# Kernel tuning notes

Measured on AMD Instinct MI355X. Metric: run time of the kernel, lower is better.

## Reference

```python
import jax, jax.numpy as jnp
import numpy as np

B, CIN, T = 32, 16, 4096
H, DEPTH, E, K = 192, 4, 4, 7
DILATIONS = (1, 2, 4, 8)
NUM_BANDS, P = 16, 8
HM = 2 * H  # mlp_ratio = 2.0
NCLS = 50
GAIN_LIMIT = 0.5
EPS = 1e-5


def _rbf_basis(num_bins, num_bands):
    freqs = jnp.linspace(0.0, 1.0, num_bins)
    centers = jnp.linspace(0.0, 1.0, num_bands)
    width = 1.5 / (num_bands - 1)
    basis = jnp.exp(-0.5 * ((freqs[None, :] - centers[:, None]) / width) ** 2)
    return basis / jnp.clip(basis.sum(-1, keepdims=True), 1e-8)


def _layernorm(x, g, b):
    m = x.mean(-1, keepdims=True)
    v = x.var(-1, keepdims=True)
    return (x - m) / jnp.sqrt(v + EPS) * g + b


def _groupnorm1(x, g, b):
    # GroupNorm(1, C): normalize over (C, T) per sample, per-channel affine
    m = x.mean((1, 2), keepdims=True)
    v = x.var((1, 2), keepdims=True)
    return (x - m) / jnp.sqrt(v + EPS) * g[None, :, None] + b[None, :, None]


def _bn_eval(x, g, b):
    # eval-mode BatchNorm1d with running_mean=0, running_var=1
    return x * (g / jnp.sqrt(1.0 + EPS))[None, :, None] + b[None, :, None]


def _gelu(x):
    return jax.nn.gelu(x, approximate=False)


def _dwconv(x, w, dilation):
    pad = (K // 2) * dilation
    return jax.lax.conv_general_dilated(
        x, w, (1,), [(pad, pad)], rhs_dilation=(dilation,),
        dimension_numbers=("NCH", "OIH", "NCH"), feature_group_count=x.shape[1])


def setup_inputs() -> dict:
    key = jax.random.key(0)
    ks = jax.random.split(key, 12)
    return {
        "x": jax.random.normal(ks[0], (B, CIN, T), jnp.float32),
        "stem_w": jax.random.normal(ks[1], (H, CIN, 3)) * 0.1,
        "stem_bn_g": jnp.ones((H,)), "stem_bn_b": jnp.zeros((H,)),
        "ln_g": jnp.ones((NUM_BANDS,)), "ln_b": jnp.zeros((NUM_BANDS,)),
        "proj_w": jax.random.normal(ks[2], (NUM_BANDS, NUM_BANDS)) * 0.25,
        "prototypes": jax.random.normal(ks[3], (P, NUM_BANDS)) * 0.02,
        "route_lib": jax.random.normal(ks[4], (P, DEPTH, E)) * 0.1,
        "gain_lib": jax.random.normal(ks[5], (P, DEPTH, H)) * 0.1,
        "norm1_g": jnp.ones((DEPTH, H)), "norm1_b": jnp.zeros((DEPTH, H)),
        "expert_w": jax.random.normal(ks[6], (DEPTH, E, H, 1, K)) * 0.2,
        "mix_w": jax.random.normal(ks[7], (DEPTH, H, H)) * (1.0 / np.sqrt(H)),
        "mix_bn_g": jnp.ones((DEPTH, H)), "mix_bn_b": jnp.zeros((DEPTH, H)),
        "norm2_g": jnp.ones((DEPTH, H)), "norm2_b": jnp.zeros((DEPTH, H)),
        "mlp_w1": jax.random.normal(ks[8], (DEPTH, HM, H)) * (1.0 / np.sqrt(H)),
        "mlp_b1": jnp.zeros((DEPTH, HM)),
        "mlp_w2": jax.random.normal(ks[9], (DEPTH, H, HM)) * (1.0 / np.sqrt(HM)),
        "mlp_b2": jnp.zeros((DEPTH, H)),
        "head_w": jax.random.normal(ks[10], (NCLS, H)) * (1.0 / np.sqrt(H)),
        "head_b": jnp.zeros((NCLS,)),
    }


def reference(x, stem_w, stem_bn_g, stem_bn_b, ln_g, ln_b, proj_w, prototypes,
              route_lib, gain_lib, norm1_g, norm1_b, expert_w, mix_w, mix_bn_g,
              mix_bn_b, norm2_g, norm2_b, mlp_w1, mlp_b1, mlp_w2, mlp_b2,
              head_w, head_b):
    # --- SpectralSummary ---
    spec = jnp.fft.rfft(x.astype(jnp.float32), axis=-1, norm="ortho")
    mag = jnp.abs(spec).mean(axis=1)                      # [B, bins]
    basis = _rbf_basis(mag.shape[-1], NUM_BANDS)          # [bands, bins]
    summary = jnp.log1p(mag) @ basis.T                    # [B, bands]
    # --- PrototypeRouter ---
    s = _layernorm(summary, ln_g, ln_b)
    rs = s @ proj_w.T
    logits = -((rs[:, None, :] - prototypes[None]) ** 2).mean(-1)  # [B, P]
    assign = jax.nn.softmax(logits * np.sqrt(NUM_BANDS), axis=-1)
    routes = jax.nn.softmax(jnp.einsum("bp,pde->bde", assign, route_lib), axis=-1)  # [B,D,E]
    gains = 1.0 + GAIN_LIMIT * jnp.tanh(jnp.einsum("bp,pdc->bdc", assign, gain_lib))  # [B,D,C]
    # --- Backbone stem ---
    z = jax.lax.conv_general_dilated(x, stem_w, (1,), [(1, 1)],
                                     dimension_numbers=("NCH", "OIH", "NCH"))
    z = _gelu(_bn_eval(z, stem_bn_g, stem_bn_b))
    # --- Routed temporal blocks ---
    for d in range(DEPTH):
        zn = _groupnorm1(z, norm1_g[d], norm1_b[d])
        pieces = jnp.stack([_dwconv(zn, expert_w[d, e], DILATIONS[e]) for e in range(E)], axis=1)  # [B,E,C,T]
        mixed = jnp.einsum("be,bect->bct", routes[:, d], pieces)
        mixed = mixed * gains[:, d][:, :, None]
        mixed = _gelu(_bn_eval(jnp.einsum("oc,bct->bot", mix_w[d], mixed), mix_bn_g[d], mix_bn_b[d]))
        z = z + mixed
        zn2 = _groupnorm1(z, norm2_g[d], norm2_b[d])
        h = _gelu(jnp.einsum("oc,bct->bot", mlp_w1[d], zn2) + mlp_b1[d][None, :, None])
        z = z + jnp.einsum("oc,bct->bot", mlp_w2[d], h) + mlp_b2[d][None, :, None]
    # --- Head: global average pool + linear ---
    pooled = z.mean(-1)
    return pooled @ head_w.T + head_b
```

## Files before the change

### kernel.cpp

```cpp
#include <hip/hip_runtime.h>
#include <math.h>

constexpr int cB = 32, cCIN = 16, cT = 4096, cH = 192, cD = 4, cE = 4, cK = 7;
constexpr int cBANDS = 16, cP = 8, cHM = 384, cNCLS = 50, cBINS = 2049;
constexpr float cEPS = 1e-5f;
constexpr int TT = 64, HALO = 24;
constexpr int ZSTR = 112;
constexpr int NTAP = 19;
constexpr float INV_SQRT2 = 0.7071067811865475f;

typedef __bf16 bf16_t;
typedef bf16_t bf16x8 __attribute__((ext_vector_type(8)));
typedef float f32x4 __attribute__((ext_vector_type(4)));

constexpr int OFFS[NTAP] = {-24,-16,-12,-8,-6,-4,-3,-2,-1,0,1,2,3,4,6,8,12,16,24};
constexpr int IDXT[cE][cK] = {
    {6, 7, 8, 9, 10, 11, 12},
    {4, 5, 7, 9, 11, 13, 14},
    {2, 3, 5, 9, 13, 15, 16},
    {0, 1, 3, 9, 15, 17, 18}};

__device__ __forceinline__ int xcd_swz(int bid) {
    return (bid & 7) * 256 + (bid >> 3);
}

__device__ __forceinline__ float fast_erf(float x) {
    float ax = fabsf(x);
    float t = 1.0f / fmaf(0.3275911f, ax, 1.0f);
    float p = t * fmaf(t, fmaf(t, fmaf(t, fmaf(t, 1.061405429f, -1.453152027f),
                                       1.421413741f), -0.284496736f), 0.254829592f);
    float e = __expf(-ax * ax);
    float r = 1.0f - p * e;
    return copysignf(r, x);
}
__device__ __forceinline__ float gelu_exact(float v) {
    return 0.5f * v * (1.0f + fast_erf(v * INV_SQRT2));
}
__device__ __forceinline__ unsigned short f2bf(float f) {
    union { float f; unsigned u; } v; v.f = f;
    unsigned r = (v.u + 0x7FFFu + ((v.u >> 16) & 1u)) >> 16;
    return (unsigned short)r;
}
__device__ __forceinline__ float bf2f(unsigned short u) {
    union { unsigned u; float f; } v; v.u = ((unsigned)u) << 16;
    return v.f;
}
__device__ __forceinline__ float bflo(unsigned u) {
    union { unsigned u; float f; } v; v.u = u << 16;
    return v.f;
}
__device__ __forceinline__ float bfhi(unsigned u) {
    union { unsigned u; float f; } v; v.u = u & 0xFFFF0000u;
    return v.f;
}

__global__ __launch_bounds__(256) void k_zero(float* __restrict__ p, int n) {
    int i = blockIdx.x * 256 + threadIdx.x;
    if (i < n) p[i] = 0.f;
}

__global__ __launch_bounds__(256) void k_cvt(const float* __restrict__ src,
                                             unsigned short* __restrict__ dst, int n) {
    int i = blockIdx.x * 256 + threadIdx.x;
    if (i < n) dst[i] = f2bf(src[i]);
}

__global__ __launch_bounds__(256) void k_cvt_w2perm(const float* __restrict__ src,
                                                    unsigned short* __restrict__ dst, int n) {
    int j = blockIdx.x * 256 + threadIdx.x;
    if (j >= n) return;
    int dd = j / (cH * cHM);
    int rem = j % (cH * cHM);
    int o = rem / cHM, m = rem % cHM;
    int wid = m / 96;
    int rr = m % 96;
    int chunk = rr / 48;
    int ii = rr % 48;
    int pos = chunk * 192 + wid * 48 + ii;
    dst[(size_t)dd * cH * cHM + (size_t)o * cHM + pos] = f2bf(src[j]);
}

__global__ __launch_bounds__(256) void k_twiddle(float2* __restrict__ tw) {
    int ls = blockIdx.x;
    int n = cT >> ls;
    int cnt = n >> 1;
    int base = cT - (cT >> ls);
    for (int p = threadIdx.x; p < cnt; p += 256) {
        float ang = -6.283185307179586f * (float)p / (float)n;
        float sv, cv;
        sincosf(ang, &sv, &cv);
        tw[base + p] = make_float2(cv, sv);
    }
}

__global__ __launch_bounds__(256) void k_fft_mag(const float* __restrict__ x,
                                                 const float2* __restrict__ tw,
                                                 float* __restrict__ mag) {
    constexpr int N2 = cT / 2;
    __shared__ float Sr[2][N2];
    __shared__ float Si[2][N2];
    int b = blockIdx.x / cCIN, c = blockIdx.x % cCIN;
    const float* xp = x + ((size_t)b * cCIN + c) * cT;
#pragma unroll
    for (int it = 0; it < N2 / 256; it++) {
        int t = threadIdx.x + it * 256;
        float2 v = *reinterpret_cast<const float2*>(&xp[2 * t]);
        Sr[0][t] = v.x; Si[0][t] = v.y;
    }
    __syncthreads();
    int cur = 0;
    for (int ls = 0; ls < 11; ls++) {
        int s = 1 << ls;
        int twb = cT - (cT >> (ls + 1));
#pragma unroll
        for (int it = 0; it < N2 / 512; it++) {
            int j = threadIdx.x + it * 256;
            int p = j >> ls;
            float2 w = tw[twb + p];
            float wr = w.x, wi = w.y;
            int ia = j, ib = j + N2 / 2;
            float ar = Sr[cur][ia], ai = Si[cur][ia];
            float br = Sr[cur][ib], bi = Si[cur][ib];
            int oa = j + (j & ~(s - 1));
            int ob = oa + s;
            Sr[cur ^ 1][oa] = ar + br;
            Si[cur ^ 1][oa] = ai + bi;
            float tr = ar - br, ti = ai - bi;
            Sr[cur ^ 1][ob] = tr * wr - ti * wi;
            Si[cur ^ 1][ob] = tr * wi + ti * wr;
        }
        __syncthreads();
        cur ^= 1;
    }
    const float scale = (1.0f / 64.0f) * (1.0f / 16.0f);
    for (int k = threadIdx.x; k <= N2; k += 256) {
        int k2 = k & (N2 - 1), km = (N2 - k) & (N2 - 1);
        float yr = Sr[cur][k2], yi = Si[cur][k2];
        float zr = Sr[cur][km], zi = Si[cur][km];
        float Ar = 0.5f * (yr + zr), Ai = 0.5f * (yi - zi);
        float Br = 0.5f * (yi + zi), Bi = -0.5f * (yr - zr);
        float wr, wi;
        if (k < N2) { float2 w = tw[k]; wr = w.x; wi = w.y; }
        else { wr = -1.f; wi = 0.f; }
        float Xr = Ar + wr * Br - wi * Bi;
        float Xi = Ai + wr * Bi + wi * Br;
        atomicAdd(&mag[b * cBINS + k], sqrtf(Xr * Xr + Xi * Xi) * scale);
    }
}

__global__ __launch_bounds__(256) void k_basis(float* __restrict__ basis) {
    __shared__ float vals[cBINS];
    __shared__ float red[256];
    int band = blockIdx.x;
    float cb = (float)band / 15.0f;
    float inv_w = 15.0f / 1.5f;
    float local = 0.f;
    for (int k = threadIdx.x; k < cBINS; k += 256) {
        float f = (float)k / 2048.0f;
        float u = (f - cb) * inv_w;
        float v = expf(-0.5f * u * u);
        vals[k] = v;
        local += v;
    }
    red[threadIdx.x] = local;
    __syncthreads();
    for (int s = 128; s > 0; s >>= 1) {
        if (threadIdx.x < s) red[threadIdx.x] += red[threadIdx.x + s];
        __syncthreads();
    }
    float inv_sum = 1.0f / fmaxf(red[0], 1e-8f);
    for (int k = threadIdx.x; k < cBINS; k += 256)
        basis[band * cBINS + k] = vals[k] * inv_sum;
}

__global__ __launch_bounds__(256) void k_summary(const float* __restrict__ mag,
                                                 const float* __restrict__ basis,
                                                 float* __restrict__ summary) {
    int b = blockIdx.x;
    float acc[cBANDS];
#pragma unroll
    for (int i = 0; i < cBANDS; i++) acc[i] = 0.f;
    for (int k = threadIdx.x; k < cBINS; k += 256) {
        float lm = log1pf(mag[b * cBINS + k]);
#pragma unroll
        for (int band = 0; band < cBANDS; band++) acc[band] += lm * basis[band * cBINS + k];
    }
    __shared__ float red[cBANDS][256];
#pragma unroll
    for (int band = 0; band < cBANDS; band++) red[band][threadIdx.x] = acc[band];
    __syncthreads();
    for (int s = 128; s > 0; s >>= 1) {
        if (threadIdx.x < s)
#pragma unroll
            for (int band = 0; band < cBANDS; band++)
                red[band][threadIdx.x] += red[band][threadIdx.x + s];
        __syncthreads();
    }
    if (threadIdx.x < cBANDS) summary[b * cBANDS + threadIdx.x] = red[threadIdx.x][0];
}

__global__ __launch_bounds__(64) void k_router(
    const float* __restrict__ summary, const float* __restrict__ ln_g,
    const float* __restrict__ ln_b, const float* __restrict__ proj_w,
    const float* __restrict__ prototypes, const float* __restrict__ route_lib,
    float* __restrict__ routes, float* __restrict__ assign_out) {
    int b = threadIdx.x;
    if (b >= cB) return;
    float s[cBANDS];
    float mean = 0.f;
#pragma unroll
    for (int i = 0; i < cBANDS; i++) { s[i] = summary[b * cBANDS + i]; mean += s[i]; }
    mean *= (1.0f / cBANDS);
    float var = 0.f;
#pragma unroll
    for (int i = 0; i < cBANDS; i++) { float d = s[i] - mean; var += d * d; }
    var *= (1.0f / cBANDS);
    float rstd = rsqrtf(var + cEPS);
#pragma unroll
    for (int i = 0; i < cBANDS; i++) s[i] = (s[i] - mean) * rstd * ln_g[i] + ln_b[i];
    float rs[cBANDS];
#pragma unroll
    for (int j = 0; j < cBANDS; j++) {
        float a = 0.f;
#pragma unroll
        for (int i = 0; i < cBANDS; i++) a += s[i] * proj_w[j * cBANDS + i];
        rs[j] = a;
    }
    float logits[cP];
    float mx = -1e30f;
#pragma unroll
    for (int p = 0; p < cP; p++) {
        float a = 0.f;
#pragma unroll
        for (int j = 0; j < cBANDS; j++) {
            float d = rs[j] - prototypes[p * cBANDS + j];
            a += d * d;
        }
        logits[p] = -(a * (1.0f / cBANDS)) * 4.0f;
        mx = fmaxf(mx, logits[p]);
    }
    float assign[cP];
    float denom = 0.f;
#pragma unroll
    for (int p = 0; p < cP; p++) { assign[p] = expf(logits[p] - mx); denom += assign[p]; }
    float invden = 1.0f / denom;
#pragma unroll
    for (int p = 0; p < cP; p++) {
        assign[p] *= invden;
        assign_out[b * cP + p] = assign[p];
    }
    for (int d = 0; d < cD; d++) {
        float r[cE];
        float rmx = -1e30f;
#pragma unroll
        for (int e = 0; e < cE; e++) {
            float a = 0.f;
#pragma unroll
            for (int p = 0; p < cP; p++) a += assign[p] * route_lib[(p * cD + d) * cE + e];
            r[e] = a;
            rmx = fmaxf(rmx, a);
        }
        float rden = 0.f;
#pragma unroll
        for (int e = 0; e < cE; e++) { r[e] = expf(r[e] - rmx); rden += r[e]; }
        float rinv = 1.0f / rden;
#pragma unroll
        for (int e = 0; e < cE; e++) routes[(b * cD + d) * cE + e] = r[e] * rinv;
    }
}

__global__ __launch_bounds__(256) void k_gains(const float* __restrict__ assign,
                                               const float* __restrict__ gain_lib,
                                               float* __restrict__ gains) {
    int i = blockIdx.x * 256 + threadIdx.x;
    if (i >= cB * cD * cH) return;
    int b = i / (cD * cH);
    int dc = i % (cD * cH);
    float a = 0.f;
#pragma unroll
    for (int p = 0; p < cP; p++) a += assign[b * cP + p] * gain_lib[p * cD * cH + dc];
    gains[i] = 1.0f + 0.5f * tanhf(a);
}

__global__ __launch_bounds__(192) void k_weff(const float* __restrict__ ew_all,
                                              const float* __restrict__ routes,
                                              unsigned short* __restrict__ weff_g) {
    int bd = blockIdx.x;
    int d = bd % cD;
    int c = threadIdx.x;
    float rte[cE];
#pragma unroll
    for (int e = 0; e < cE; e++) rte[e] = routes[bd * cE + e];
    float acc[NTAP];
#pragma unroll
    for (int o = 0; o < NTAP; o++) acc[o] = 0.f;
#pragma unroll
    for (int e = 0; e < cE; e++) {
#pragma unroll
        for (int k = 0; k < cK; k++)
            acc[IDXT[e][k]] += rte[e] * ew_all[(((size_t)d * cE + e) * cH + c) * cK + k];
    }
    unsigned short* dst = weff_g + ((size_t)bd * cH + c) * 20;
#pragma unroll
    for (int o = 0; o < NTAP; o++) dst[o] = f2bf(acc[o]);
    dst[NTAP] = 0;
}

constexpr int STT = 256;
__global__ __launch_bounds__(256) void k_stem(const float* __restrict__ x,
                                              const float* __restrict__ stem_w,
                                              const float* __restrict__ bn_g,
                                              const float* __restrict__ bn_b,
                                              unsigned short* __restrict__ z,
                                              float* __restrict__ sums_out) {
    __shared__ float xs[cCIN][STT + 2];
    __shared__ float ws[cH * cCIN * 3];
    int blk = blockIdx.x;
    int b = blk / (cT / STT);
    int t0 = (blk % (cT / STT)) * STT;
    for (int i = threadIdx.x; i < cH * cCIN * 3; i += 256) ws[i] = stem_w[i];
    for (int i = threadIdx.x; i < cCIN * (STT + 2); i += 256) {
        int c = i / (STT + 2), tt = i % (STT + 2);
        int gt = t0 + tt - 1;
        xs[c][tt] = (gt >= 0 && gt < cT) ? x[((size_t)b * cCIN + c) * cT + gt] : 0.f;
    }
    __syncthreads();
    int tt = threadIdx.x;
    float xv[cCIN][3];
#pragma unroll
    for (int c = 0; c < cCIN; c++)
#pragma unroll
        for (int k = 0; k < 3; k++) xv[c][k] = xs[c][tt + k];
    int gt = t0 + tt;
    float bnrs = rsqrtf(1.0f + cEPS);
    float s = 0.f, q = 0.f;
    for (int h = 0; h < cH; h++) {
        const float* w = &ws[h * cCIN * 3];
        float acc = 0.f;
#pragma unroll
        for (int c = 0; c < cCIN; c++)
#pragma unroll
            for (int k = 0; k < 3; k++) acc += xv[c][k] * w[c * 3 + k];
        float v = acc * (bn_g[h] * bnrs) + bn_b[h];
        unsigned short rb = f2bf(gelu_exact(v));
        float res = bf2f(rb);
        z[((size_t)b * cH + h) * cT + gt] = rb;
        s += res; q += res * res;
    }
#pragma unroll
    for (int off = 32; off > 0; off >>= 1) { s += __shfl_down(s, off); q += __shfl_down(q, off); }
    if ((threadIdx.x & 63) == 0) {
        atomicAdd(&sums_out[b * 2], s);
        atomicAdd(&sums_out[b * 2 + 1], q);
    }
}

__global__ __launch_bounds__(256, 2) void k_block1(
    const unsigned short* __restrict__ zin, unsigned short* __restrict__ zout,
    const float* __restrict__ sums_in, float* __restrict__ sums_out,
    const float* __restrict__ g1, const float* __restrict__ b1,
    const unsigned short* __restrict__ weff_g, const unsigned short* __restrict__ mwb,
    const float* __restrict__ mg, const float* __restrict__ mb,
    const float* __restrict__ gains, int d) {
    __shared__ unsigned short zn[cH][ZSTR];
    __shared__ unsigned short mxT[TT][200];
    int blk = xcd_swz(blockIdx.x);
    int b = blk / (cT / TT);
    int t0 = (blk % (cT / TT)) * TT;
    int tid = threadIdx.x;
    const float invN = 1.0f / (float)(cH * cT);
    float mean = sums_in[b * 2] * invN;
    float var = sums_in[b * 2 + 1] * invN - mean * mean;
    float rstd = rsqrtf(var + cEPS);
    constexpr int S_ITERS = cH * 28 / 256;
    bool interior = (t0 >= HALO) && (t0 + TT + HALO <= cT);
    if (interior) {
#pragma unroll
        for (int it = 0; it < S_ITERS; it++) {
            int i = tid + it * 256;
            int c = i / 28, tt = (i % 28) * 4;
            int gt = t0 + tt - HALO;
            float gc = g1[c], bc = b1[c];
            ushort4 v = *reinterpret_cast<const ushort4*>(&zin[((size_t)b * cH + c) * cT + gt]);
            ushort4 pk;
            pk.x = f2bf((bf2f(v.x) - mean) * rstd * gc + bc);
            pk.y = f2bf((bf2f(v.y) - mean) * rstd * gc + bc);
            pk.z = f2bf((bf2f(v.z) - mean) * rstd * gc + bc);
            pk.w = f2bf((bf2f(v.w) - mean) * rstd * gc + bc);
            *reinterpret_cast<ushort4*>(&zn[c][tt]) = pk;
        }
    } else {
#pragma unroll
        for (int it = 0; it < S_ITERS; it++) {
            int i = tid + it * 256;
            int c = i / 28, tt = (i % 28) * 4;
            int gt = t0 + tt - HALO;
            float gc = g1[c], bc = b1[c];
            const unsigned short* zp = &zin[((size_t)b * cH + c) * cT];
            float n0 = (gt + 0 >= 0 && gt + 0 < cT) ? (bf2f(zp[gt + 0]) - mean) * rstd * gc + bc : 0.f;
            float n1 = (gt + 1 >= 0 && gt + 1 < cT) ? (bf2f(zp[gt + 1]) - mean) * rstd * gc + bc : 0.f;
            float n2 = (gt + 2 >= 0 && gt + 2 < cT) ? (bf2f(zp[gt + 2]) - mean) * rstd * gc + bc : 0.f;
            float n3 = (gt + 3 >= 0 && gt + 3 < cT) ? (bf2f(zp[gt + 3]) - mean) * rstd * gc + bc : 0.f;
            ushort4 pk;
            pk.x = f2bf(n0); pk.y = f2bf(n1); pk.z = f2bf(n2); pk.w = f2bf(n3);
            *reinterpret_cast<ushort4*>(&zn[c][tt]) = pk;
        }
    }
    int lane = tid & 63, wid = tid >> 6;
    int lrow = lane & 15;
    int lk8 = (lane >> 4) << 3;
    int r0 = (lane >> 4) << 2;
    int mbase = wid * 48;
    float res[3][4][4];
#pragma unroll
    for (int mt = 0; mt < 3; mt++)
#pragma unroll
        for (int nt = 0; nt < 4; nt++)
#pragma unroll
            for (int r = 0; r < 4; r++)
                res[mt][nt][r] = bf2f(zin[((size_t)b * cH + mbase + mt * 16 + r0 + r) * cT +
                                         t0 + nt * 16 + lrow]);
    __syncthreads();
    if (tid < cH) {
        int c = tid;
        const unsigned short* wp = weff_g + ((size_t)(b * cD + d) * cH + c) * 20;
        float wv[NTAP];
#pragma unroll
        for (int o = 0; o < NTAP; o++) wv[o] = bf2f(wp[o]);
        float g = gains[((size_t)b * cD + d) * cH + c];
        float win[ZSTR];
#pragma unroll
        for (int v = 0; v < 14; v++) {
            bf16x8 w8 = *reinterpret_cast<const bf16x8*>(&zn[c][8 * v]);
#pragma unroll
            for (int u = 0; u < 8; u++) win[8 * v + u] = (float)w8[u];
        }
#pragma unroll
        for (int t = 0; t < TT; t++) {
            float a = 0.f;
#pragma unroll
            for (int o = 0; o < NTAP; o++)
                a = fmaf(wv[o], win[t + HALO + OFFS[o]], a);
            mxT[t][c] = f2bf(a * g);
        }
    }
    __syncthreads();
    f32x4 acc[3][4];
#pragma unroll
    for (int mt = 0; mt < 3; mt++)
#pragma unroll
        for (int nt = 0; nt < 4; nt++)
#pragma unroll
            for (int r = 0; r < 4; r++) acc[mt][nt][r] = 0.f;
#pragma unroll
    for (int kk = 0; kk < 6; kk++) {
        int k0 = kk * 32 + lk8;
        bf16x8 a0 = *reinterpret_cast<const bf16x8*>(&mwb[(size_t)(mbase + lrow) * cH + k0]);
        bf16x8 a1 = *reinterpret_cast<const bf16x8*>(&mwb[(size_t)(mbase + 16 + lrow) * cH + k0]);
        bf16x8 a2 = *reinterpret_cast<const bf16x8*>(&mwb[(size_t)(mbase + 32 + lrow) * cH + k0]);
#pragma unroll
        for (int nt = 0; nt < 4; nt++) {
            bf16x8 bf = *reinterpret_cast<const bf16x8*>(&mxT[nt * 16 + lrow][k0]);
            acc[0][nt] = __builtin_amdgcn_mfma_f32_16x16x32_bf16(a0, bf, acc[0][nt], 0, 0, 0);
            acc[1][nt] = __builtin_amdgcn_mfma_f32_16x16x32_bf16(a1, bf, acc[1][nt], 0, 0, 0);
            acc[2][nt] = __builtin_amdgcn_mfma_f32_16x16x32_bf16(a2, bf, acc[2][nt], 0, 0, 0);
        }
    }
    float bnrs = rsqrtf(1.0f + cEPS);
    float s = 0.f, q = 0.f;
#pragma unroll
    for (int mt = 0; mt < 3; mt++) {
#pragma unroll
        for (int nt = 0; nt < 4; nt++) {
#pragma unroll
            for (int r = 0; r < 4; r++) {
                int o = mbase + mt * 16 + r0 + r;
                int t = t0 + nt * 16 + lrow;
                size_t idx = ((size_t)b * cH + o) * cT + t;
                unsigned short vb = f2bf(res[mt][nt][r] +
                                         gelu_exact(acc[mt][nt][r] * (mg[o] * bnrs) + mb[o]));
                float val = bf2f(vb);
                zout[idx] = vb;
                s += val; q += val * val;
            }
        }
    }
#pragma unroll
    for (int off = 32; off > 0; off >>= 1) { s += __shfl_down(s, off); q += __shfl_down(q, off); }
    if (lane == 0) {
        atomicAdd(&sums_out[b * 2], s);
        atomicAdd(&sums_out[b * 2 + 1], q);
    }
}

__global__ __launch_bounds__(256, 2) void k_block2(
    unsigned short* __restrict__ z, const float* __restrict__ sums_in,
    float* __restrict__ sums_out,
    const float* __restrict__ g2, const float* __restrict__ b2,
    const unsigned short* __restrict__ w1b, const float* __restrict__ bb1,
    const unsigned short* __restrict__ w2p, const float* __restrict__ bb2) {
    __shared__ unsigned short znT[TT][200];
    __shared__ unsigned short hT[TT][200];
    int blk = xcd_swz(blockIdx.x);
    int b = blk / (cT / TT);
    int t0 = (blk % (cT / TT)) * TT;
    const float invN = 1.0f / (float)(cH * cT);
    float mean = sums_in[b * 2] * invN;
    float var = sums_in[b * 2 + 1] * invN - mean * mean;
    float rstd = rsqrtf(var + cEPS);
    constexpr int S_ITERS = cH * (TT / 4) / 256;
#pragma unroll
    for (int it = 0; it < S_ITERS; it++) {
        int i = threadIdx.x + it * 256;
        int c = i >> 4, t4 = (i & 15) << 2;
        ushort4 v = *reinterpret_cast<const ushort4*>(&z[((size_t)b * cH + c) * cT + t0 + t4]);
        float gc = g2[c], bc = b2[c];
        znT[t4 + 0][c] = f2bf((bf2f(v.x) - mean) * rstd * gc + bc);
        znT[t4 + 1][c] = f2bf((bf2f(v.y) - mean) * rstd * gc + bc);
        znT[t4 + 2][c] = f2bf((bf2f(v.z) - mean) * rstd * gc + bc);
        znT[t4 + 3][c] = f2bf((bf2f(v.w) - mean) * rstd * gc + bc);
    }
    int lane = threadIdx.x & 63, wid = threadIdx.x >> 6;
    int lrow = lane & 15;
    int lk8 = (lane >> 4) << 3;
    int r0 = (lane >> 4) << 2;
    int obase = wid * 48;
    float res[3][4][4];
#pragma unroll
    for (int mt = 0; mt < 3; mt++)
#pragma unroll
        for (int nt = 0; nt < 4; nt++)
#pragma unroll
            for (int r = 0; r < 4; r++)
                res[mt][nt][r] = bf2f(z[((size_t)b * cH + obase + mt * 16 + r0 + r) * cT +
                                        t0 + nt * 16 + lrow]);
    __syncthreads();
    f32x4 acc2[3][4];
#pragma unroll
    for (int mt = 0; mt < 3; mt++) {
#pragma unroll
        for (int r = 0; r < 4; r++) {
            float bv = bb2[obase + mt * 16 + r0 + r];
            acc2[mt][0][r] = bv; acc2[mt][1][r] = bv; acc2[mt][2][r] = bv; acc2[mt][3][r] = bv;
        }
    }
#pragma unroll
    for (int chunk = 0; chunk < 2; chunk++) {
        int mbase = wid * 96 + chunk * 48;
        f32x4 acc1[3][4];
#pragma unroll
        for (int mt = 0; mt < 3; mt++) {
#pragma unroll
            for (int r = 0; r < 4; r++) {
                float bv = bb1[mbase + mt * 16 + r0 + r];
                acc1[mt][0][r] = bv; acc1[mt][1][r] = bv; acc1[mt][2][r] = bv; acc1[mt][3][r] = bv;
            }
        }
#pragma unroll
        for (int kk = 0; kk < 6; kk++) {
            int k0 = kk * 32 + lk8;
            bf16x8 a0 = *reinterpret_cast<const bf16x8*>(&w1b[(size_t)(mbase + lrow) * cH + k0]);
            bf16x8 a1 = *reinterpret_cast<const bf16x8*>(&w1b[(size_t)(mbase + 16 + lrow) * cH + k0]);
            bf16x8 a2 = *reinterpret_cast<const bf16x8*>(&w1b[(size_t)(mbase + 32 + lrow) * cH + k0]);
#pragma unroll
            for (int nt = 0; nt < 4; nt++) {
                bf16x8 bf = *reinterpret_cast<const bf16x8*>(&znT[nt * 16 + lrow][k0]);
                acc1[0][nt] = __builtin_amdgcn_mfma_f32_16x16x32_bf16(a0, bf, acc1[0][nt], 0, 0, 0);
                acc1[1][nt] = __builtin_amdgcn_mfma_f32_16x16x32_bf16(a1, bf, acc1[1][nt], 0, 0, 0);
                acc1[2][nt] = __builtin_amdgcn_mfma_f32_16x16x32_bf16(a2, bf, acc1[2][nt], 0, 0, 0);
            }
        }
#pragma unroll
        for (int mt = 0; mt < 3; mt++) {
            int o0 = wid * 48 + mt * 16 + r0;
#pragma unroll
            for (int nt = 0; nt < 4; nt++) {
                int t = nt * 16 + lrow;
                ushort4 pk;
                pk.x = f2bf(gelu_exact(acc1[mt][nt][0]));
                pk.y = f2bf(gelu_exact(acc1[mt][nt][1]));
                pk.z = f2bf(gelu_exact(acc1[mt][nt][2]));
                pk.w = f2bf(gelu_exact(acc1[mt][nt][3]));
                *reinterpret_cast<ushort4*>(&hT[t][o0]) = pk;
            }
        }
        __syncthreads();
#pragma unroll
        for (int kk = 0; kk < 6; kk++) {
            int kl = kk * 32 + lk8;
            int kg = chunk * 192 + kl;
            bf16x8 a0 = *reinterpret_cast<const bf16x8*>(&w2p[(size_t)(obase + lrow) * cHM + kg]);
            bf16x8 a1 = *reinterpret_cast<const bf16x8*>(&w2p[(size_t)(obase + 16 + lrow) * cHM + kg]);
            bf16x8 a2 = *reinterpret_cast<const bf16x8*>(&w2p[(size_t)(obase + 32 + lrow) * cHM + kg]);
#pragma unroll
            for (int nt = 0; nt < 4; nt++) {
                bf16x8 bf = *reinterpret_cast<const bf16x8*>(&hT[nt * 16 + lrow][kl]);
                acc2[0][nt] = __builtin_amdgcn_mfma_f32_16x16x32_bf16(a0, bf, acc2[0][nt], 0, 0, 0);
                acc2[1][nt] = __builtin_amdgcn_mfma_f32_16x16x32_bf16(a1, bf, acc2[1][nt], 0, 0, 0);
                acc2[2][nt] = __builtin_amdgcn_mfma_f32_16x16x32_bf16(a2, bf, acc2[2][nt], 0, 0, 0);
            }
        }
        if (chunk == 0) __syncthreads();
    }
    float s = 0.f, q = 0.f;
#pragma unroll
    for (int mt = 0; mt < 3; mt++) {
#pragma unroll
        for (int nt = 0; nt < 4; nt++) {
#pragma unroll
            for (int r = 0; r < 4; r++) {
                int o = obase + mt * 16 + r0 + r;
                int t = t0 + nt * 16 + lrow;
                size_t idx = ((size_t)b * cH + o) * cT + t;
                unsigned short vb = f2bf(res[mt][nt][r] + acc2[mt][nt][r]);
                float val = bf2f(vb);
                z[idx] = vb;
                s += val; q += val * val;
            }
        }
    }
#pragma unroll
    for (int off = 32; off > 0; off >>= 1) { s += __shfl_down(s, off); q += __shfl_down(q, off); }
    if (lane == 0) {
        atomicAdd(&sums_out[b * 2], s);
        atomicAdd(&sums_out[b * 2 + 1], q);
    }
}

__global__ __launch_bounds__(256) void k_pool(const unsigned short* __restrict__ z,
                                              float* __restrict__ pooled) {
    int bh = blockIdx.x;
    const unsigned short* zp = z + (size_t)bh * cT;
    float s = 0.f;
#pragma unroll
    for (int it = 0; it < 2; it++) {
        uint4 v = *reinterpret_cast<const uint4*>(&zp[(threadIdx.x + it * 256) * 8]);
        s += bflo(v.x) + bfhi(v.x) + bflo(v.y) + bfhi(v.y) +
             bflo(v.z) + bfhi(v.z) + bflo(v.w) + bfhi(v.w);
    }
    __shared__ float red[256];
    red[threadIdx.x] = s;
    __syncthreads();
    for (int st = 128; st > 0; st >>= 1) {
        if (threadIdx.x < st) red[threadIdx.x] += red[threadIdx.x + st];
        __syncthreads();
    }
    if (threadIdx.x == 0) pooled[bh] = red[0] * (1.0f / cT);
}

__global__ __launch_bounds__(256) void k_head(const float* __restrict__ pooled,
                                              const float* __restrict__ hw,
                                              const float* __restrict__ hb,
                                              float* __restrict__ out) {
    int i = blockIdx.x * 256 + threadIdx.x;
    if (i >= cB * cNCLS) return;
    int b = i / cNCLS, n = i % cNCLS;
    float acc = hb[n];
    const float* pw = pooled + b * cH;
    const float* wr = hw + n * cH;
    for (int h = 0; h < cH; h++) acc += pw[h] * wr[h];
    out[i] = acc;
}

extern "C" void kernel_launch(void* const* d_in, const int* in_sizes, int n_in,
                              void* d_out, int out_size, void* d_ws, size_t ws_size,
                              hipStream_t stream) {
    const float* x          = (const float*)d_in[0];
    const float* stem_w     = (const float*)d_in[1];
    const float* stem_bn_g  = (const float*)d_in[2];
    const float* stem_bn_b  = (const float*)d_in[3];
    const float* ln_g       = (const float*)d_in[4];
    const float* ln_b       = (const float*)d_in[5];
    const float* proj_w     = (const float*)d_in[6];
    const float* prototypes = (const float*)d_in[7];
    const float* route_lib  = (const float*)d_in[8];
    const float* gain_lib   = (const float*)d_in[9];
    const float* norm1_g    = (const float*)d_in[10];
    const float* norm1_b    = (const float*)d_in[11];
    const float* expert_w   = (const float*)d_in[12];
    const float* mix_w      = (const float*)d_in[13];
    const float* mix_bn_g   = (const float*)d_in[14];
    const float* mix_bn_b   = (const float*)d_in[15];
    const float* norm2_g    = (const float*)d_in[16];
    const float* norm2_b    = (const float*)d_in[17];
    const float* mlp_w1     = (const float*)d_in[18];
    const float* mlp_b1     = (const float*)d_in[19];
    const float* mlp_w2     = (const float*)d_in[20];
    const float* mlp_b2     = (const float*)d_in[21];
    const float* head_w     = (const float*)d_in[22];
    const float* head_b     = (const float*)d_in[23];

    float* ws = (float*)d_ws;
    size_t off = 0;
    const size_t ZN = (size_t)cB * cH * cT;
    unsigned short* zA = (unsigned short*)(ws + off); off += ZN / 2;
    unsigned short* zB = (unsigned short*)(ws + off); off += ZN / 2;
    float* mag     = ws + off; off += (size_t)cB * cBINS;
    float* sums    = ws + off; off += 9 * cB * 2;
    float* basis   = ws + off; off += (size_t)cBANDS * cBINS;
    float* summary = ws + off; off += cB * cBANDS;
    float* routes  = ws + off; off += cB * cD * cE;
    float* assign  = ws + off; off += cB * cP;
    float* gains   = ws + off; off += (size_t)cB * cD * cH;
    float* pooled  = ws + off; off += cB * cH;
    float2* tw     = (float2*)(ws + off); off += 2 * (cT - 1) + 2;
    unsigned short* mixb = (unsigned short*)(ws + off); off += (size_t)cD * cH * cH / 2;
    unsigned short* w1b  = (unsigned short*)(ws + off); off += (size_t)cD * cHM * cH / 2;
    unsigned short* w2b  = (unsigned short*)(ws + off); off += (size_t)cD * cH * cHM / 2;
    unsigned short* weff = (unsigned short*)(ws + off); off += (size_t)cB * cD * cH * 20 / 2;

    int nz = cB * cBINS + 9 * cB * 2;
    k_zero<<<(nz + 255) / 256, 256, 0, stream>>>(mag, nz);

    k_cvt<<<(cD * cH * cH + 255) / 256, 256, 0, stream>>>(mix_w, mixb, cD * cH * cH);
    k_cvt<<<(cD * cHM * cH + 255) / 256, 256, 0, stream>>>(mlp_w1, w1b, cD * cHM * cH);
    k_cvt_w2perm<<<(cD * cH * cHM + 255) / 256, 256, 0, stream>>>(mlp_w2, w2b, cD * cH * cHM);

    k_twiddle<<<12, 256, 0, stream>>>(tw);
    k_fft_mag<<<cB * cCIN, 256, 0, stream>>>(x, tw, mag);
    k_basis<<<cBANDS, 256, 0, stream>>>(basis);
    k_summary<<<cB, 256, 0, stream>>>(mag, basis, summary);
    k_router<<<1, 64, 0, stream>>>(summary, ln_g, ln_b, proj_w, prototypes,
                                   route_lib, routes, assign);
    k_gains<<<(cB * cD * cH + 255) / 256, 256, 0, stream>>>(assign, gain_lib, gains);
    k_weff<<<cB * cD, 192, 0, stream>>>(expert_w, routes, weff);

    k_stem<<<cB * (cT / STT), 256, 0, stream>>>(x, stem_w, stem_bn_g, stem_bn_b, zA,
                                                sums + 0 * cB * 2);

    unsigned short* zi = zA;
    unsigned short* zo = zB;
    for (int d = 0; d < cD; d++) {
        k_block1<<<cB * (cT / TT), 256, 0, stream>>>(
            zi, zo, sums + (size_t)(2 * d) * cB * 2, sums + (size_t)(2 * d + 1) * cB * 2,
            norm1_g + d * cH, norm1_b + d * cH,
            weff, mixb + (size_t)d * cH * cH,
            mix_bn_g + d * cH, mix_bn_b + d * cH, gains, d);
        k_block2<<<cB * (cT / TT), 256, 0, stream>>>(
            zo, sums + (size_t)(2 * d + 1) * cB * 2, sums + (size_t)(2 * d + 2) * cB * 2,
            norm2_g + d * cH, norm2_b + d * cH,
            w1b + (size_t)d * cHM * cH, mlp_b1 + d * cHM,
            w2b + (size_t)d * cH * cHM, mlp_b2 + d * cH);
        unsigned short* t = zi; zi = zo; zo = t;
    }

    k_pool<<<cB * cH, 256, 0, stream>>>(zi, pooled);
    k_head<<<(cB * cNCLS + 255) / 256, 256, 0, stream>>>(pooled, head_w, head_b,
                                                         (float*)d_out);
}
```

Before: 1.053 ms.

## Restructure MLP block kernel to 512 threads with full hidden tile in LDS

The MLP kernel now launches 512 threads (8 waves). Each wave computes 48 of the 384 hidden channels in a single pass and writes them into an enlarged LDS hidden buffer. The second GEMM then splits the work as 4 output-channel groups by 2 time halves. This removes the two-chunk loop with its extra barriers and the permuted w2 layout, so w2 now uses the plain conversion kernel. It raises LDS use per block (about 75 KB) and drops the 2-blocks-per-CU launch bound, which may change occupancy and register pressure.

```diff
diff --git a/kernel.cpp b/kernel.cpp
--- a/kernel.cpp
+++ b/kernel.cpp
@@ -63,21 +63,6 @@
                                              unsigned short* __restrict__ dst, int n) {
     int i = blockIdx.x * 256 + threadIdx.x;
     if (i < n) dst[i] = f2bf(src[i]);
-}
-
-__global__ __launch_bounds__(256) void k_cvt_w2perm(const float* __restrict__ src,
-                                                    unsigned short* __restrict__ dst, int n) {
-    int j = blockIdx.x * 256 + threadIdx.x;
-    if (j >= n) return;
-    int dd = j / (cH * cHM);
-    int rem = j % (cH * cHM);
-    int o = rem / cHM, m = rem % cHM;
-    int wid = m / 96;
-    int rr = m % 96;
-    int chunk = rr / 48;
-    int ii = rr % 48;
-    int pos = chunk * 192 + wid * 48 + ii;
-    dst[(size_t)dd * cH * cHM + (size_t)o * cHM + pos] = f2bf(src[j]);
 }
 
 __global__ __launch_bounds__(256) void k_twiddle(float2* __restrict__ tw) {
@@ -493,14 +478,14 @@
     }
 }
 
-__global__ __launch_bounds__(256, 2) void k_block2(
+__global__ __launch_bounds__(512) void k_block2(
     unsigned short* __restrict__ z, const float* __restrict__ sums_in,
     float* __restrict__ sums_out,
     const float* __restrict__ g2, const float* __restrict__ b2,
     const unsigned short* __restrict__ w1b, const float* __restrict__ bb1,
-    const unsigned short* __restrict__ w2p, const float* __restrict__ bb2) {
+    const unsigned short* __restrict__ w2b, const float* __restrict__ bb2) {
     __shared__ unsigned short znT[TT][200];
-    __shared__ unsigned short hT[TT][200];
+    __shared__ unsigned short hT[TT][392];
     int blk = xcd_swz(blockIdx.x);
     int b = blk / (cT / TT);
     int t0 = (blk % (cT / TT)) * TT;
@@ -508,10 +493,10 @@
     float mean = sums_in[b * 2] * invN;
     float var = sums_in[b * 2 + 1] * invN - mean * mean;
     float rstd = rsqrtf(var + cEPS);
-    constexpr int S_ITERS = cH * (TT / 4) / 256;
+    constexpr int S_ITERS = cH * (TT / 4) / 512;
 #pragma unroll
     for (int it = 0; it < S_ITERS; it++) {
-        int i = threadIdx.x + it * 256;
+        int i = threadIdx.x + it * 512;
         int c = i >> 4, t4 = (i & 15) << 2;
         ushort4 v = *reinterpret_cast<const ushort4*>(&z[((size_t)b * cH + c) * cT + t0 + t4]);
         float gc = g2[c], bc = b2[c];
@@ -524,93 +509,90 @@
     int lrow = lane & 15;
     int lk8 = (lane >> 4) << 3;
     int r0 = (lane >> 4) << 2;
-    int obase = wid * 48;
-    float res[3][4][4];
+    int mg = wid >> 1, ng = wid & 1;
+    int obase = mg * 48;
+    int tb = ng * 32;
+    float res[3][2][4];
 #pragma unroll
     for (int mt = 0; mt < 3; mt++)
 #pragma unroll
-        for (int nt = 0; nt < 4; nt++)
+        for (int nt = 0; nt < 2; nt++)
 #pragma unroll
             for (int r = 0; r < 4; r++)
                 res[mt][nt][r] = bf2f(z[((size_t)b * cH + obase + mt * 16 + r0 + r) * cT +
-                                        t0 + nt * 16 + lrow]);
-    __syncthreads();
-    f32x4 acc2[3][4];
+                                        t0 + tb + nt * 16 + lrow]);
+    __syncthreads();
+    int w1base = wid * 48;
+    f32x4 acc1[3][4];
+#pragma unroll
+    for (int mt = 0; mt < 3; mt++) {
+#pragma unroll
+        for (int r = 0; r < 4; r++) {
+            float bv = bb1[w1base + mt * 16 + r0 + r];
+            acc1[mt][0][r] = bv; acc1[mt][1][r] = bv; acc1[mt][2][r] = bv; acc1[mt][3][r] = bv;
+        }
+    }
+#pragma unroll
+    for (int kk = 0; kk < 6; kk++) {
+        int k0 = kk * 32 + lk8;
+        bf16x8 a0 = *reinterpret_cast<const bf16x8*>(&w1b[(size_t)(w1base + lrow) * cH + k0]);
+        bf16x8 a1 = *reinterpret_cast<const bf16x8*>(&w1b[(size_t)(w1base + 16 + lrow) * cH + k0]);
+        bf16x8 a2 = *reinterpret_cast<const bf16x8*>(&w1b[(size_t)(w1base + 32 + lrow) * cH + k0]);
+#pragma unroll
+        for (int nt = 0; nt < 4; nt++) {
+            bf16x8 bf = *reinterpret_cast<const bf16x8*>(&znT[nt * 16 + lrow][k0]);
+            acc1[0][nt] = __builtin_amdgcn_mfma_f32_16x16x32_bf16(a0, bf, acc1[0][nt], 0, 0, 0);
+            acc1[1][nt] = __builtin_amdgcn_mfma_f32_16x16x32_bf16(a1, bf, acc1[1][nt], 0, 0, 0);
+            acc1[2][nt] = __builtin_amdgcn_mfma_f32_16x16x32_bf16(a2, bf, acc1[2][nt], 0, 0, 0);
+        }
+    }
+#pragma unroll
+    for (int mt = 0; mt < 3; mt++) {
+        int o0 = w1base + mt * 16 + r0;
+#pragma unroll
+        for (int nt = 0; nt < 4; nt++) {
+            int t = nt * 16 + lrow;
+            ushort4 pk;
+            pk.x = f2bf(gelu_exact(acc1[mt][nt][0]));
+            pk.y = f2bf(gelu_exact(acc1[mt][nt][1]));
+            pk.z = f2bf(gelu_exact(acc1[mt][nt][2]));
+            pk.w = f2bf(gelu_exact(acc1[mt][nt][3]));
+            *reinterpret_cast<ushort4*>(&hT[t][o0]) = pk;
+        }
+    }
+    __syncthreads();
+    f32x4 acc2[3][2];
 #pragma unroll
     for (int mt = 0; mt < 3; mt++) {
 #pragma unroll
         for (int r = 0; r < 4; r++) {
             float bv = bb2[obase + mt * 16 + r0 + r];
-            acc2[mt][0][r] = bv; acc2[mt][1][r] = bv; acc2[mt][2][r] = bv; acc2[mt][3][r] = bv;
-        }
-    }
-#pragma unroll
-    for (int chunk = 0; chunk < 2; chunk++) {
-        int mbase = wid * 96 + chunk * 48;
-        f32x4 acc1[3][4];
-#pragma unroll
-        for (int mt = 0; mt < 3; mt++) {
-#pragma unroll
-            for (int r = 0; r < 4; r++) {
-                float bv = bb1[mbase + mt * 16 + r0 + r];
-                acc1[mt][0][r] = bv; acc1[mt][1][r] = bv; acc1[mt][2][r] = bv; acc1[mt][3][r] = bv;
-            }
-        }
-#pragma unroll
-        for (int kk = 0; kk < 6; kk++) {
-            int k0 = kk * 32 + lk8;
-            bf16x8 a0 = *reinterpret_cast<const bf16x8*>(&w1b[(size_t)(mbase + lrow) * cH + k0]);
-            bf16x8 a1 = *reinterpret_cast<const bf16x8*>(&w1b[(size_t)(mbase + 16 + lrow) * cH + k0]);
-            bf16x8 a2 = *reinterpret_cast<const bf16x8*>(&w1b[(size_t)(mbase + 32 + lrow) * cH + k0]);
-#pragma unroll
-            for (int nt = 0; nt < 4; nt++) {
-                bf16x8 bf = *reinterpret_cast<const bf16x8*>(&znT[nt * 16 + lrow][k0]);
-                acc1[0][nt] = __builtin_amdgcn_mfma_f32_16x16x32_bf16(a0, bf, acc1[0][nt], 0, 0, 0);
-                acc1[1][nt] = __builtin_amdgcn_mfma_f32_16x16x32_bf16(a1, bf, acc1[1][nt], 0, 0, 0);
-                acc1[2][nt] = __builtin_amdgcn_mfma_f32_16x16x32_bf16(a2, bf, acc1[2][nt], 0, 0, 0);
-            }
-        }
-#pragma unroll
-        for (int mt = 0; mt < 3; mt++) {
-            int o0 = wid * 48 + mt * 16 + r0;
-#pragma unroll
-            for (int nt = 0; nt < 4; nt++) {
-                int t = nt * 16 + lrow;
-                ushort4 pk;
-                pk.x = f2bf(gelu_exact(acc1[mt][nt][0]));
-                pk.y = f2bf(gelu_exact(acc1[mt][nt][1]));
-                pk.z = f2bf(gelu_exact(acc1[mt][nt][2]));
-                pk.w = f2bf(gelu_exact(acc1[mt][nt][3]));
-                *reinterpret_cast<ushort4*>(&hT[t][o0]) = pk;
-            }
-        }
-        __syncthreads();
-#pragma unroll
-        for (int kk = 0; kk < 6; kk++) {
-            int kl = kk * 32 + lk8;
-            int kg = chunk * 192 + kl;
-            bf16x8 a0 = *reinterpret_cast<const bf16x8*>(&w2p[(size_t)(obase + lrow) * cHM + kg]);
-            bf16x8 a1 = *reinterpret_cast<const bf16x8*>(&w2p[(size_t)(obase + 16 + lrow) * cHM + kg]);
-            bf16x8 a2 = *reinterpret_cast<const bf16x8*>(&w2p[(size_t)(obase + 32 + lrow) * cHM + kg]);
-#pragma unroll
-            for (int nt = 0; nt < 4; nt++) {
-                bf16x8 bf = *reinterpret_cast<const bf16x8*>(&hT[nt * 16 + lrow][kl]);
-                acc2[0][nt] = __builtin_amdgcn_mfma_f32_16x16x32_bf16(a0, bf, acc2[0][nt], 0, 0, 0);
-                acc2[1][nt] = __builtin_amdgcn_mfma_f32_16x16x32_bf16(a1, bf, acc2[1][nt], 0, 0, 0);
-                acc2[2][nt] = __builtin_amdgcn_mfma_f32_16x16x32_bf16(a2, bf, acc2[2][nt], 0, 0, 0);
-            }
-        }
-        if (chunk == 0) __syncthreads();
+            acc2[mt][0][r] = bv; acc2[mt][1][r] = bv;
+        }
+    }
+#pragma unroll
+    for (int kk = 0; kk < 12; kk++) {
+        int k0 = kk * 32 + lk8;
+        bf16x8 a0 = *reinterpret_cast<const bf16x8*>(&w2b[(size_t)(obase + lrow) * cHM + k0]);
+        bf16x8 a1 = *reinterpret_cast<const bf16x8*>(&w2b[(size_t)(obase + 16 + lrow) * cHM + k0]);
+        bf16x8 a2 = *reinterpret_cast<const bf16x8*>(&w2b[(size_t)(obase + 32 + lrow) * cHM + k0]);
+#pragma unroll
+        for (int nt = 0; nt < 2; nt++) {
+            bf16x8 bf = *reinterpret_cast<const bf16x8*>(&hT[tb + nt * 16 + lrow][k0]);
+            acc2[0][nt] = __builtin_amdgcn_mfma_f32_16x16x32_bf16(a0, bf, acc2[0][nt], 0, 0, 0);
+            acc2[1][nt] = __builtin_amdgcn_mfma_f32_16x16x32_bf16(a1, bf, acc2[1][nt], 0, 0, 0);
+            acc2[2][nt] = __builtin_amdgcn_mfma_f32_16x16x32_bf16(a2, bf, acc2[2][nt], 0, 0, 0);
+        }
     }
     float s = 0.f, q = 0.f;
 #pragma unroll
     for (int mt = 0; mt < 3; mt++) {
 #pragma unroll
-        for (int nt = 0; nt < 4; nt++) {
+        for (int nt = 0; nt < 2; nt++) {
 #pragma unroll
             for (int r = 0; r < 4; r++) {
                 int o = obase + mt * 16 + r0 + r;
-                int t = t0 + nt * 16 + lrow;
+                int t = t0 + tb + nt * 16 + lrow;
                 size_t idx = ((size_t)b * cH + o) * cT + t;
                 unsigned short vb = f2bf(res[mt][nt][r] + acc2[mt][nt][r]);
                 float val = bf2f(vb);
@@ -714,7 +696,7 @@
 
     k_cvt<<<(cD * cH * cH + 255) / 256, 256, 0, stream>>>(mix_w, mixb, cD * cH * cH);
     k_cvt<<<(cD * cHM * cH + 255) / 256, 256, 0, stream>>>(mlp_w1, w1b, cD * cHM * cH);
-    k_cvt_w2perm<<<(cD * cH * cHM + 255) / 256, 256, 0, stream>>>(mlp_w2, w2b, cD * cH * cHM);
+    k_cvt<<<(cD * cH * cHM + 255) / 256, 256, 0, stream>>>(mlp_w2, w2b, cD * cH * cHM);
 
     k_twiddle<<<12, 256, 0, stream>>>(tw);
     k_fft_mag<<<cB * cCIN, 256, 0, stream>>>(x, tw, mag);
@@ -736,7 +718,7 @@
             norm1_g + d * cH, norm1_b + d * cH,
             weff, mixb + (size_t)d * cH * cH,
             mix_bn_g + d * cH, mix_bn_b + d * cH, gains, d);
-        k_block2<<<cB * (cT / TT), 256, 0, stream>>>(
+        k_block2<<<cB * (cT / TT), 512, 0, stream>>>(
             zo, sums + (size_t)(2 * d + 1) * cB * 2, sums + (size_t)(2 * d + 2) * cB * 2,
             norm2_g + d * cH, norm2_b + d * cH,
             w1b + (size_t)d * cHM * cH, mlp_b1 + d * cHM,
```

After: 1.316 ms. 1.25x slower.
